# Kernel optimization log

Hardware: AMD Instinct MI355X
Metric: run time of the kernel (lower is better)

## Reference

```python
import jax, jax.numpy as jnp
import numpy as np

N = 50000          # nodes
E = 3_200_000      # edges (radius-graph topology, avg degree ~64)
C = 10             # node channels
ED = 4             # edge_dim: [dist, dx, dy, food_flag]
H = 16             # message hidden dim
RADIUS = 0.05
ACC_SCALE = 0.005
MAX_VEL = 0.02
EDGES_TO_STAY_ALIVE = 3
CONSUMPTION_EDGES_REQUIRED = 3
NOISE_SCALE = 0.004


def setup_inputs() -> dict:
    key = jax.random.key(0)
    ks = jax.random.split(key, 10)
    pos = jax.random.uniform(ks[0], (N, 2), minval=-1.0, maxval=1.0)
    vel = jax.random.uniform(ks[1], (N, 2), minval=-MAX_VEL, maxval=MAX_VEL)
    # column 4: 1.0 = living cell, 0.0 = food node
    is_cell = (jax.random.uniform(ks[2], (N,)) > 0.2).astype(jnp.float32)
    hidden = jax.random.normal(ks[3], (N, C - 5)) * 0.1
    x = jnp.concatenate([pos, vel, is_cell[:, None], hidden], axis=1)  # [N,10]
    src = jax.random.randint(ks[4], (E,), 0, N)
    dst = jax.random.randint(ks[5], (E,), 0, N)
    noise = jax.random.uniform(ks[6], (N, 2))  # uniform [0,1), mapped to [-1,1) inside
    W_edge = jax.random.normal(ks[7], (ED, H)) * 0.3
    W_src = jax.random.normal(ks[8], (C, H)) * 0.3
    b1 = jnp.zeros((H,), jnp.float32)
    W_out = jax.random.normal(ks[9], (H, 4)) * 0.3
    b2 = jnp.zeros((4,), jnp.float32)
    return dict(x=x, src=src, dst=dst, noise=noise, W_edge=W_edge,
                W_src=W_src, b1=b1, W_out=W_out, b2=b2)


def reference(x, src, dst, noise, W_edge, W_src, b1, W_out, b2):
    pos = x[:, :2]
    vel = x[:, 2:4]
    cell = x[:, 4]
    c_mask = (cell == 1.0).astype(x.dtype)          # [N]

    # ---- edge attributes of the (dynamic) radius graph ----
    d = pos[src] - pos[dst]                          # [E,2] gather
    dist = jnp.sqrt(jnp.sum(d * d, axis=1) + 1e-12)  # [E]
    food_flag = cell[src]                            # 0 for food-source edges
    edge_attr = jnp.concatenate([dist[:, None], d, food_flag[:, None]], axis=1)  # [E,4]

    # ---- message passing: per-edge MLP + scatter-sum + node readout ----
    m = jax.nn.relu(edge_attr @ W_edge + x[src] @ W_src + b1)     # [E,H]
    agg = jax.ops.segment_sum(m, dst, num_segments=N)             # [N,H]
    h = jnp.tanh(agg @ W_out + b2) * c_mask[:, None]              # [N,4], masked as in update_graph

    # ---- velocity / position update ----
    acc = h[:, :2] * ACC_SCALE
    new_vel = jnp.clip(vel + acc, -MAX_VEL, MAX_VEL)
    new_pos = pos + new_vel                                       # wrap_around = False
    vel_noisy = new_vel + (noise * 2.0 - 1.0) * NOISE_SCALE * c_mask[:, None]
    new_x = jnp.concatenate(
        [new_pos, vel_noisy, cell[:, None], h[:, 2:], x[:, 7:]], axis=1)  # [N,10]

    # ---- costs / stats ----
    eps = 1e-6
    border_mask = (jnp.abs(new_pos) > 1.0).astype(x.dtype)        # [N,2]
    border_cost = jnp.sum(jnp.log(jnp.abs(new_pos) + eps) * border_mask)
    food_edge = (food_flag == 0.0)
    visible_food = food_edge.sum()
    mean_food_dist = jnp.sum(dist * food_edge.astype(x.dtype))

    # ---- node removal masks (jit-safe: return keep mask instead of slicing) ----
    deg = jax.ops.segment_sum(jnp.ones_like(dist), dst, num_segments=N)
    dead = (cell == 1.0) & (deg < EDGES_TO_STAY_ALIVE)
    consume_e = (dist < RADIUS) & (cell[src] == 1.0) & (cell[dst] == 0.0)
    cdeg = jax.ops.segment_sum(consume_e.astype(x.dtype), dst, num_segments=N)
    consumed = (cell == 0.0) & (cdeg >= CONSUMPTION_EDGES_REQUIRED)
    keep_mask = ~(dead | consumed)

    velocity_bonus = jnp.mean(jnp.abs(new_vel), axis=0)           # [2]
    dead_cost = dead.sum()
    food_reward = consumed.sum()
    return (new_x, keep_mask, velocity_bonus, border_cost, food_reward,
            dead_cost, visible_food, mean_food_dist)
```

## Files before the change

kernel.cpp:

```cpp
#include <hip/hip_runtime.h>
#include <math.h>

#define NN 50000
#define NE 3200000

#define NTILE 196
#define TSZ   256
#define CAP   20480
#define SCB   250
#define SCH   12800

static constexpr float ACC_SCALE   = 0.005f;
static constexpr float MAX_VEL     = 0.02f;
static constexpr float NOISE_SCALE = 0.004f;
static constexpr float RADIUS      = 0.05f;

#define OUT_NEWX   0
#define OUT_KEEP   500000
#define OUT_SCAL   550000

#define WS_NI   0
#define WS_S2   200704
#define WS_CUR  1003520
#define WS_BK   1003776

__global__ __launch_bounds__(256) void k1_prep(
    const float* __restrict__ x,
    const float* __restrict__ W_edge,
    const float* __restrict__ W_src,
    const float* __restrict__ b1,
    float4* __restrict__ nodeinfo,
    float* __restrict__ s2,
    int* __restrict__ cursor,
    float* __restrict__ out_scalars)
{
    int n = blockIdx.x * 256 + threadIdx.x;
    if (blockIdx.x == 0) {
        if (threadIdx.x < 7) out_scalars[threadIdx.x] = 0.0f;
        if (threadIdx.x < NTILE) cursor[threadIdx.x] = threadIdx.x * CAP;
    }
    if (n >= NN) return;

    float xr[10];
#pragma unroll
    for (int c = 0; c < 10; ++c) xr[c] = x[n * 10 + c];
    float cell = xr[4];

    nodeinfo[n] = make_float4(xr[0], xr[1], cell, 0.0f);

#pragma unroll
    for (int j = 0; j < 16; ++j) {
        float v = fmaf(cell, W_edge[48 + j], b1[j]);
#pragma unroll
        for (int c = 0; c < 10; ++c) v = fmaf(xr[c], W_src[c * 16 + j], v);
        s2[n * 16 + j] = v;
    }
}

__global__ __launch_bounds__(256) void k_scatter(
    const int* __restrict__ src,
    const int* __restrict__ dst,
    int* __restrict__ cursor,
    unsigned* __restrict__ bucket)
{
    __shared__ int hist[NTILE];
    __shared__ int base[NTILE];
    __shared__ int lcur[NTILE];
    int tid = threadIdx.x;
    for (int i = tid; i < NTILE; i += 256) { hist[i] = 0; lcur[i] = 0; }
    __syncthreads();

    int e0 = blockIdx.x * SCH;
#pragma unroll 4
    for (int j = 0; j < SCH / 256; ++j) {
        int d = dst[e0 + j * 256 + tid];
        atomicAdd(&hist[d >> 8], 1);
    }
    __syncthreads();
    for (int i = tid; i < NTILE; i += 256)
        base[i] = atomicAdd(&cursor[i], hist[i]);
    __syncthreads();

    for (int j = 0; j < SCH / 256; ++j) {
        int e = e0 + j * 256 + tid;
        int d = dst[e];
        int s = src[e];
        int b = d >> 8;
        int pos = base[b] + atomicAdd(&lcur[b], 1);
        if (pos < (b + 1) * CAP)
            bucket[pos] = (unsigned)s | ((unsigned)(d & 255) << 16);
    }
}

__global__ __launch_bounds__(512) void k_agg(
    const float* __restrict__ x,
    const float* __restrict__ noise,
    const float* __restrict__ W_edge,
    const float* __restrict__ W_out,
    const float* __restrict__ b2,
    const float4* __restrict__ nodeinfo,
    const float* __restrict__ s2,
    const int* __restrict__ cursor,
    const unsigned* __restrict__ bucket,
    float* __restrict__ out,
    float* __restrict__ out_scalars)
{
    __shared__ float  sAcc[TSZ][4];
    __shared__ int    sDeg[TSZ];
    __shared__ float4 sNI[TSZ];
    __shared__ float  sRed[8][8];

    int t = blockIdx.x;
    int tid = threadIdx.x;

    if (tid < TSZ) {
        int g = t * TSZ + tid;
        sNI[tid] = (g < NN) ? nodeinfo[g] : make_float4(9e9f, 9e9f, -1.f, 0.f);
        sAcc[tid][0] = 0.f; sAcc[tid][1] = 0.f;
        sAcc[tid][2] = 0.f; sAcc[tid][3] = 0.f;
        sDeg[tid] = 0;
    }

    float w0[16], w1[16], w2[16], woa[16], wob[16], woc[16], wod[16];
#pragma unroll
    for (int k = 0; k < 16; ++k) {
        w0[k] = W_edge[k];
        w1[k] = W_edge[16 + k];
        w2[k] = W_edge[32 + k];
        woa[k] = W_out[k * 4 + 0];
        wob[k] = W_out[k * 4 + 1];
        woc[k] = W_out[k * 4 + 2];
        wod[k] = W_out[k * 4 + 3];
    }
    __syncthreads();

    int cnt = cursor[t] - t * CAP;
    if (cnt > CAP) cnt = CAP;

    float vis = 0.f, fd = 0.f;
    for (int i = tid; i < cnt; i += 512) {
        unsigned e = bucket[t * CAP + i];
        int s  = e & 0xFFFF;
        int dl = (e >> 16) & 0xFF;
        float4 ns = nodeinfo[s];
        float4 nt = sNI[dl];
        float dx = ns.x - nt.x;
        float dy = ns.y - nt.y;
        float dist = sqrtf(fmaf(dx, dx, fmaf(dy, dy, 1e-12f)));

        bool food0 = (ns.z == 0.0f);
        vis += food0 ? 1.f : 0.f;
        fd  += food0 ? dist : 0.f;

        bool consume = (dist < RADIUS) && (ns.z == 1.0f) && (nt.z == 0.0f);
        atomicAdd(&sDeg[dl], consume ? 65537 : 1);

        const float4* sv4 = (const float4*)(s2 + (size_t)s * 16);
        float4 q0 = sv4[0], q1 = sv4[1], q2 = sv4[2], q3 = sv4[3];
        float sv[16] = { q0.x, q0.y, q0.z, q0.w, q1.x, q1.y, q1.z, q1.w,
                         q2.x, q2.y, q2.z, q2.w, q3.x, q3.y, q3.z, q3.w };

        float v0 = 0.f, v1 = 0.f, v2 = 0.f, v3 = 0.f;
#pragma unroll
        for (int k = 0; k < 16; ++k) {
            float m = fmaf(dist, w0[k], fmaf(dx, w1[k], fmaf(dy, w2[k], sv[k])));
            m = fmaxf(m, 0.0f);
            v0 = fmaf(m, woa[k], v0);
            v1 = fmaf(m, wob[k], v1);
            v2 = fmaf(m, woc[k], v2);
            v3 = fmaf(m, wod[k], v3);
        }
        atomicAdd(&sAcc[dl][0], v0);
        atomicAdd(&sAcc[dl][1], v1);
        atomicAdd(&sAcc[dl][2], v2);
        atomicAdd(&sAcc[dl][3], v3);
    }
    __syncthreads();

    float avx = 0.f, avy = 0.f, bc = 0.f, deadf = 0.f, consf = 0.f;
    int n = t * TSZ + tid;
    if (tid < TSZ && n < NN) {
        float cell = x[n * 10 + 4];
        float cm = (cell == 1.0f) ? 1.0f : 0.0f;
        float h0 = tanhf(sAcc[tid][0] + b2[0]) * cm;
        float h1 = tanhf(sAcc[tid][1] + b2[1]) * cm;
        float h2 = tanhf(sAcc[tid][2] + b2[2]) * cm;
        float h3 = tanhf(sAcc[tid][3] + b2[3]) * cm;

        float px = x[n * 10 + 0], py = x[n * 10 + 1];
        float vx = x[n * 10 + 2], vy = x[n * 10 + 3];

        float nvx = fminf(fmaxf(fmaf(h0, ACC_SCALE, vx), -MAX_VEL), MAX_VEL);
        float nvy = fminf(fmaxf(fmaf(h1, ACC_SCALE, vy), -MAX_VEL), MAX_VEL);
        float npx = px + nvx;
        float npy = py + nvy;

        float vnx = nvx + (noise[n * 2 + 0] * 2.0f - 1.0f) * NOISE_SCALE * cm;
        float vny = nvy + (noise[n * 2 + 1] * 2.0f - 1.0f) * NOISE_SCALE * cm;

        float* row = out + OUT_NEWX + (size_t)n * 10;
        row[0] = npx;  row[1] = npy;
        row[2] = vnx;  row[3] = vny;
        row[4] = cell; row[5] = h2;  row[6] = h3;
        row[7] = x[n * 10 + 7];
        row[8] = x[n * 10 + 8];
        row[9] = x[n * 10 + 9];

        float apx = fabsf(npx), apy = fabsf(npy);
        if (apx > 1.0f) bc += logf(apx + 1e-6f);
        if (apy > 1.0f) bc += logf(apy + 1e-6f);

        int dp = sDeg[tid];
        int deg  = dp & 0xFFFF;
        int cdeg = dp >> 16;
        bool dead = (cell == 1.0f) && (deg < 3);
        bool cons = (cell == 0.0f) && (cdeg >= 3);
        out[OUT_KEEP + n] = (dead || cons) ? 0.0f : 1.0f;
        deadf = dead ? 1.0f : 0.0f;
        consf = cons ? 1.0f : 0.0f;
        avx = fabsf(nvx) * (1.0f / NN);
        avy = fabsf(nvy) * (1.0f / NN);
    }

    float r[7] = { avx, avy, bc, consf, deadf, vis, fd };
#pragma unroll
    for (int q = 0; q < 7; ++q) {
#pragma unroll
        for (int off = 32; off > 0; off >>= 1)
            r[q] += __shfl_down(r[q], off);
    }
    int lane = tid & 63, wv = tid >> 6;
    if (lane == 0) {
#pragma unroll
        for (int q = 0; q < 7; ++q) sRed[wv][q] = r[q];
    }
    __syncthreads();
    if (tid == 0) {
#pragma unroll
        for (int q = 0; q < 7; ++q) {
            float acc = 0.f;
#pragma unroll
            for (int wq = 0; wq < 8; ++wq) acc += sRed[wq][q];
            atomicAdd(&out_scalars[q], acc);
        }
    }
}

extern "C" void kernel_launch(void* const* d_in, const int* in_sizes, int n_in,
                              void* d_out, int out_size, void* d_ws, size_t ws_size,
                              hipStream_t stream) {
    const float* x      = (const float*)d_in[0];
    const int*   src    = (const int*)  d_in[1];
    const int*   dst    = (const int*)  d_in[2];
    const float* noise  = (const float*)d_in[3];
    const float* W_edge = (const float*)d_in[4];
    const float* W_src  = (const float*)d_in[5];
    const float* b1     = (const float*)d_in[6];
    const float* W_out  = (const float*)d_in[7];
    const float* b2     = (const float*)d_in[8];

    float* ws = (float*)d_ws;
    float4*   nodeinfo = (float4*)(ws + WS_NI);
    float*    s2       = ws + WS_S2;
    int*      cursor   = (int*)(ws + WS_CUR);
    unsigned* bucket   = (unsigned*)(ws + WS_BK);

    float* out         = (float*)d_out;
    float* out_scalars = out + OUT_SCAL;

    k1_prep<<<NTILE, 256, 0, stream>>>(
        x, W_edge, W_src, b1, nodeinfo, s2, cursor, out_scalars);

    k_scatter<<<SCB, 256, 0, stream>>>(src, dst, cursor, bucket);

    k_agg<<<NTILE, 512, 0, stream>>>(
        x, noise, W_edge, W_out, b2, nodeinfo, s2, cursor, bucket,
        out, out_scalars);
}
```

Measured before the change: 245.6 us.

## Stage scatter writes in LDS and split tile aggregation across eight slices

The scatter kernel now stages edges per destination tile in shared memory and flushes them in 64-entry chunks, so bucket writes are coalesced instead of scattered. Tiles grow to 512 nodes, and each tile's edge list is split across 8 blocks, raising the aggregation grid from 196 to 784 blocks for better occupancy. Partial accumulators and degrees go to workspace and are summed in a new finalize kernel. This adds an extra launch, extra global traffic for the partials, and many barriers per scatter round, and per-tile staging could overflow the 320-entry buffer under skewed inputs.

Result: slower. 300.2 us (+22.2%).

```diff
diff --git a/kernel.cpp b/kernel.cpp
--- a/kernel.cpp
+++ b/kernel.cpp
@@ -4,25 +4,29 @@
 #define NN 50000
 #define NE 3200000
 
-#define NTILE 196
-#define TSZ   256
-#define CAP   20480
+#define NT    98
+#define TSZ   512
+#define CAP   34816
 #define SCB   250
 #define SCH   12800
+#define SROUNDS 50
+#define STCAP 320
+#define NSL   8
 
 static constexpr float ACC_SCALE   = 0.005f;
 static constexpr float MAX_VEL     = 0.02f;
 static constexpr float NOISE_SCALE = 0.004f;
 static constexpr float RADIUS      = 0.05f;
 
-#define OUT_NEWX   0
 #define OUT_KEEP   500000
 #define OUT_SCAL   550000
 
-#define WS_NI   0
-#define WS_S2   200704
-#define WS_CUR  1003520
-#define WS_BK   1003776
+#define WS_NI    0
+#define WS_S2    200704
+#define WS_GCUR  1003520
+#define WS_BK    1003648
+#define WS_PACC  4415616
+#define WS_PDEG  6021248
 
 __global__ __launch_bounds__(256) void k1_prep(
     const float* __restrict__ x,
@@ -31,13 +35,13 @@
     const float* __restrict__ b1,
     float4* __restrict__ nodeinfo,
     float* __restrict__ s2,
-    int* __restrict__ cursor,
+    int* __restrict__ gcur,
     float* __restrict__ out_scalars)
 {
     int n = blockIdx.x * 256 + threadIdx.x;
     if (blockIdx.x == 0) {
         if (threadIdx.x < 7) out_scalars[threadIdx.x] = 0.0f;
-        if (threadIdx.x < NTILE) cursor[threadIdx.x] = threadIdx.x * CAP;
+        if (threadIdx.x < NT) gcur[threadIdx.x] = threadIdx.x * CAP;
     }
     if (n >= NN) return;
 
@@ -60,65 +64,135 @@
 __global__ __launch_bounds__(256) void k_scatter(
     const int* __restrict__ src,
     const int* __restrict__ dst,
-    int* __restrict__ cursor,
+    int* __restrict__ gcur,
     unsigned* __restrict__ bucket)
 {
-    __shared__ int hist[NTILE];
-    __shared__ int base[NTILE];
-    __shared__ int lcur[NTILE];
+    extern __shared__ unsigned smem[];
+    unsigned* stage = smem;
+    int* hist   = (int*)(smem + NT * STCAP);
+    int* gbase  = hist  + NT;
+    int* lofs   = gbase + NT;
+    int* scnt   = lofs  + NT;
+    int* wl_t   = scnt  + NT;
+    int* wl_n   = wl_t  + NT;
+    int* wl_g   = wl_n  + NT;
+    int* wl_cnt = wl_g  + NT;
+
     int tid = threadIdx.x;
-    for (int i = tid; i < NTILE; i += 256) { hist[i] = 0; lcur[i] = 0; }
+    for (int i = tid; i < NT; i += 256) { hist[i] = 0; lofs[i] = 0; scnt[i] = 0; }
     __syncthreads();
 
     int e0 = blockIdx.x * SCH;
+
 #pragma unroll 4
-    for (int j = 0; j < SCH / 256; ++j) {
-        int d = dst[e0 + j * 256 + tid];
-        atomicAdd(&hist[d >> 8], 1);
-    }
-    __syncthreads();
-    for (int i = tid; i < NTILE; i += 256)
-        base[i] = atomicAdd(&cursor[i], hist[i]);
-    __syncthreads();
-
-    for (int j = 0; j < SCH / 256; ++j) {
-        int e = e0 + j * 256 + tid;
-        int d = dst[e];
-        int s = src[e];
-        int b = d >> 8;
-        int pos = base[b] + atomicAdd(&lcur[b], 1);
-        if (pos < (b + 1) * CAP)
-            bucket[pos] = (unsigned)s | ((unsigned)(d & 255) << 16);
+    for (int r = 0; r < SROUNDS; ++r) {
+        int d = dst[e0 + r * 256 + tid];
+        atomicAdd(&hist[d >> 9], 1);
+    }
+    __syncthreads();
+    if (tid < NT) gbase[tid] = atomicAdd(&gcur[tid], hist[tid]);
+
+    int eA = e0 + tid;
+    int dA = dst[eA],        sA = src[eA];
+    int dB = dst[eA + 256],  sB = src[eA + 256];
+
+    for (int r = 0; r < SROUNDS; ++r) {
+        int dc = dA, sc = sA;
+        dA = dB; sA = sB;
+        int en = eA + (r + 2) * 256;
+        if (r + 2 < SROUNDS) { dB = dst[en]; sB = src[en]; }
+
+        if (tid == 0) *wl_cnt = 0;
+        {
+            int t = dc >> 9;
+            unsigned entry = (unsigned)sc | ((unsigned)(dc & 511) << 16);
+            int pos = atomicAdd(&scnt[t], 1);
+            stage[t * STCAP + pos] = entry;
+        }
+        __syncthreads();
+
+        if (tid < NT) {
+            int c = scnt[tid];
+            int nf = (c >> 6) << 6;
+            if (nf) {
+                int slot = atomicAdd(wl_cnt, 1);
+                wl_t[slot] = tid;
+                wl_n[slot] = nf;
+                wl_g[slot] = gbase[tid] + lofs[tid];
+                lofs[tid] += nf;
+            }
+        }
+        __syncthreads();
+
+        int nw = *wl_cnt;
+        for (int w = 0; w < nw; ++w) {
+            int t = wl_t[w], n = wl_n[w], g0 = wl_g[w];
+            int glim = (t + 1) * CAP;
+            for (int idx = tid; idx < n; idx += 256) {
+                int g = g0 + idx;
+                if (g < glim) bucket[g] = stage[t * STCAP + idx];
+            }
+        }
+        __syncthreads();
+
+        if (tid < nw) {
+            int t = wl_t[tid], n = wl_n[tid];
+            int c = scnt[t];
+            for (int j = 0; j + n < c; ++j)
+                stage[t * STCAP + j] = stage[t * STCAP + n + j];
+            scnt[t] = c - n;
+        }
+        __syncthreads();
+    }
+
+    if (tid == 0) *wl_cnt = 0;
+    __syncthreads();
+    if (tid < NT) {
+        int c = scnt[tid];
+        if (c) {
+            int slot = atomicAdd(wl_cnt, 1);
+            wl_t[slot] = tid;
+            wl_n[slot] = c;
+            wl_g[slot] = gbase[tid] + lofs[tid];
+        }
+    }
+    __syncthreads();
+    int nw = *wl_cnt;
+    for (int w = 0; w < nw; ++w) {
+        int t = wl_t[w], n = wl_n[w], g0 = wl_g[w];
+        int glim = (t + 1) * CAP;
+        for (int idx = tid; idx < n; idx += 256) {
+            int g = g0 + idx;
+            if (g < glim) bucket[g] = stage[t * STCAP + idx];
+        }
     }
 }
 
-__global__ __launch_bounds__(512) void k_agg(
-    const float* __restrict__ x,
-    const float* __restrict__ noise,
+__global__ __launch_bounds__(256) void k_agg(
     const float* __restrict__ W_edge,
     const float* __restrict__ W_out,
-    const float* __restrict__ b2,
     const float4* __restrict__ nodeinfo,
     const float* __restrict__ s2,
-    const int* __restrict__ cursor,
+    const int* __restrict__ gcur,
     const unsigned* __restrict__ bucket,
-    float* __restrict__ out,
+    float4* __restrict__ pacc,
+    int* __restrict__ pdeg,
     float* __restrict__ out_scalars)
 {
     __shared__ float  sAcc[TSZ][4];
     __shared__ int    sDeg[TSZ];
     __shared__ float4 sNI[TSZ];
-    __shared__ float  sRed[8][8];
-
-    int t = blockIdx.x;
+    __shared__ float  sRed[4][2];
+
+    int t   = blockIdx.x >> 3;
+    int sl  = blockIdx.x & 7;
     int tid = threadIdx.x;
 
-    if (tid < TSZ) {
-        int g = t * TSZ + tid;
-        sNI[tid] = (g < NN) ? nodeinfo[g] : make_float4(9e9f, 9e9f, -1.f, 0.f);
-        sAcc[tid][0] = 0.f; sAcc[tid][1] = 0.f;
-        sAcc[tid][2] = 0.f; sAcc[tid][3] = 0.f;
-        sDeg[tid] = 0;
+    for (int j = tid; j < TSZ; j += 256) {
+        int g = t * TSZ + j;
+        sNI[j] = (g < NN) ? nodeinfo[g] : make_float4(9e9f, 9e9f, -1.f, 0.f);
+        sAcc[j][0] = 0.f; sAcc[j][1] = 0.f; sAcc[j][2] = 0.f; sAcc[j][3] = 0.f;
+        sDeg[j] = 0;
     }
 
     float w0[16], w1[16], w2[16], woa[16], wob[16], woc[16], wod[16];
@@ -134,14 +208,18 @@
     }
     __syncthreads();
 
-    int cnt = cursor[t] - t * CAP;
+    int cnt = gcur[t] - t * CAP;
     if (cnt > CAP) cnt = CAP;
+    int cs = (cnt + NSL - 1) / NSL;
+    int i0 = sl * cs;
+    int i1 = min(i0 + cs, cnt);
 
     float vis = 0.f, fd = 0.f;
-    for (int i = tid; i < cnt; i += 512) {
+#pragma unroll 2
+    for (int i = i0 + tid; i < i1; i += 256) {
         unsigned e = bucket[t * CAP + i];
         int s  = e & 0xFFFF;
-        int dl = (e >> 16) & 0xFF;
+        int dl = (e >> 16) & 0x1FF;
         float4 ns = nodeinfo[s];
         float4 nt = sNI[dl];
         float dx = ns.x - nt.x;
@@ -177,15 +255,60 @@
     }
     __syncthreads();
 
+    for (int j = tid; j < TSZ; j += 256) {
+        int o = sl * (NT * TSZ) + t * TSZ + j;
+        pacc[o] = make_float4(sAcc[j][0], sAcc[j][1], sAcc[j][2], sAcc[j][3]);
+        pdeg[o] = sDeg[j];
+    }
+
+#pragma unroll
+    for (int off = 32; off > 0; off >>= 1) {
+        vis += __shfl_down(vis, off);
+        fd  += __shfl_down(fd,  off);
+    }
+    int lane = tid & 63, wv = tid >> 6;
+    if (lane == 0) { sRed[wv][0] = vis; sRed[wv][1] = fd; }
+    __syncthreads();
+    if (tid == 0) {
+        float a = 0.f, b = 0.f;
+#pragma unroll
+        for (int wq = 0; wq < 4; ++wq) { a += sRed[wq][0]; b += sRed[wq][1]; }
+        atomicAdd(&out_scalars[5], a);
+        atomicAdd(&out_scalars[6], b);
+    }
+}
+
+__global__ __launch_bounds__(256) void k_final(
+    const float* __restrict__ x,
+    const float* __restrict__ noise,
+    const float* __restrict__ b2,
+    const float4* __restrict__ pacc,
+    const int* __restrict__ pdeg,
+    float* __restrict__ out,
+    float* __restrict__ out_scalars)
+{
+    __shared__ float sRed[4][5];
+    int n = blockIdx.x * 256 + threadIdx.x;
+    int tid = threadIdx.x;
+
     float avx = 0.f, avy = 0.f, bc = 0.f, deadf = 0.f, consf = 0.f;
-    int n = t * TSZ + tid;
-    if (tid < TSZ && n < NN) {
+
+    if (n < NN) {
+        float a0 = 0.f, a1 = 0.f, a2 = 0.f, a3 = 0.f;
+        int dp = 0;
+#pragma unroll
+        for (int sl = 0; sl < NSL; ++sl) {
+            float4 q = pacc[sl * (NT * TSZ) + n];
+            a0 += q.x; a1 += q.y; a2 += q.z; a3 += q.w;
+            dp += pdeg[sl * (NT * TSZ) + n];
+        }
+
         float cell = x[n * 10 + 4];
         float cm = (cell == 1.0f) ? 1.0f : 0.0f;
-        float h0 = tanhf(sAcc[tid][0] + b2[0]) * cm;
-        float h1 = tanhf(sAcc[tid][1] + b2[1]) * cm;
-        float h2 = tanhf(sAcc[tid][2] + b2[2]) * cm;
-        float h3 = tanhf(sAcc[tid][3] + b2[3]) * cm;
+        float h0 = tanhf(a0 + b2[0]) * cm;
+        float h1 = tanhf(a1 + b2[1]) * cm;
+        float h2 = tanhf(a2 + b2[2]) * cm;
+        float h3 = tanhf(a3 + b2[3]) * cm;
 
         float px = x[n * 10 + 0], py = x[n * 10 + 1];
         float vx = x[n * 10 + 2], vy = x[n * 10 + 3];
@@ -198,7 +321,7 @@
         float vnx = nvx + (noise[n * 2 + 0] * 2.0f - 1.0f) * NOISE_SCALE * cm;
         float vny = nvy + (noise[n * 2 + 1] * 2.0f - 1.0f) * NOISE_SCALE * cm;
 
-        float* row = out + OUT_NEWX + (size_t)n * 10;
+        float* row = out + (size_t)n * 10;
         row[0] = npx;  row[1] = npy;
         row[2] = vnx;  row[3] = vny;
         row[4] = cell; row[5] = h2;  row[6] = h3;
@@ -210,7 +333,6 @@
         if (apx > 1.0f) bc += logf(apx + 1e-6f);
         if (apy > 1.0f) bc += logf(apy + 1e-6f);
 
-        int dp = sDeg[tid];
         int deg  = dp & 0xFFFF;
         int cdeg = dp >> 16;
         bool dead = (cell == 1.0f) && (deg < 3);
@@ -222,9 +344,9 @@
         avy = fabsf(nvy) * (1.0f / NN);
     }
 
-    float r[7] = { avx, avy, bc, consf, deadf, vis, fd };
-#pragma unroll
-    for (int q = 0; q < 7; ++q) {
+    float r[5] = { avx, avy, bc, consf, deadf };
+#pragma unroll
+    for (int q = 0; q < 5; ++q) {
 #pragma unroll
         for (int off = 32; off > 0; off >>= 1)
             r[q] += __shfl_down(r[q], off);
@@ -232,15 +354,13 @@
     int lane = tid & 63, wv = tid >> 6;
     if (lane == 0) {
 #pragma unroll
-        for (int q = 0; q < 7; ++q) sRed[wv][q] = r[q];
+        for (int q = 0; q < 5; ++q) sRed[wv][q] = r[q];
     }
     __syncthreads();
     if (tid == 0) {
 #pragma unroll
-        for (int q = 0; q < 7; ++q) {
-            float acc = 0.f;
-#pragma unroll
-            for (int wq = 0; wq < 8; ++wq) acc += sRed[wq][q];
+        for (int q = 0; q < 5; ++q) {
+            float acc = sRed[0][q] + sRed[1][q] + sRed[2][q] + sRed[3][q];
             atomicAdd(&out_scalars[q], acc);
         }
     }
@@ -262,18 +382,23 @@
     float* ws = (float*)d_ws;
     float4*   nodeinfo = (float4*)(ws + WS_NI);
     float*    s2       = ws + WS_S2;
-    int*      cursor   = (int*)(ws + WS_CUR);
+    int*      gcur     = (int*)(ws + WS_GCUR);
     unsigned* bucket   = (unsigned*)(ws + WS_BK);
+    float4*   pacc     = (float4*)(ws + WS_PACC);
+    int*      pdeg     = (int*)(ws + WS_PDEG);
 
     float* out         = (float*)d_out;
     float* out_scalars = out + OUT_SCAL;
 
-    k1_prep<<<NTILE, 256, 0, stream>>>(
-        x, W_edge, W_src, b1, nodeinfo, s2, cursor, out_scalars);
-
-    k_scatter<<<SCB, 256, 0, stream>>>(src, dst, cursor, bucket);
-
-    k_agg<<<NTILE, 512, 0, stream>>>(
-        x, noise, W_edge, W_out, b2, nodeinfo, s2, cursor, bucket,
-        out, out_scalars);
+    k1_prep<<<196, 256, 0, stream>>>(
+        x, W_edge, W_src, b1, nodeinfo, s2, gcur, out_scalars);
+
+    size_t scatter_lds = (size_t)(NT * STCAP + 7 * NT + 1) * sizeof(unsigned);
+    k_scatter<<<SCB, 256, scatter_lds, stream>>>(src, dst, gcur, bucket);
+
+    k_agg<<<NT * NSL, 256, 0, stream>>>(
+        W_edge, W_out, nodeinfo, s2, gcur, bucket, pacc, pdeg, out_scalars);
+
+    k_final<<<196, 256, 0, stream>>>(
+        x, noise, b2, pacc, pdeg, out, out_scalars);
 }
```
